# Kernel tuning notes

Measured on AMD Instinct MI355X. Metric: run time of the kernel, lower is better.

## Reference

```python
import jax, jax.numpy as jnp
import numpy as np

B, N, D, H = 2, 2048, 2048, 16
HD = D // H  # head_dim = 128
EPS = 1e-06

def rmsnorm(x, w, eps=EPS):
    xf = x.astype(jnp.float32)
    y = xf * jax.lax.rsqrt(jnp.mean(xf * xf, axis=-1, keepdims=True) + eps)
    return y.astype(x.dtype) * w

def rope_apply(x, freqs, num_heads):
    # x: [B, S, D]; freqs: [S, 1, HD//2, 2] = (cos, sin) of complex rotation
    b, s, d = x.shape
    hd = d // num_heads
    xr = x.reshape(b, s, num_heads, hd // 2, 2)
    x0, x1 = xr[..., 0], xr[..., 1]
    fr, fi = freqs[..., 0], freqs[..., 1]  # broadcast [S,1,HD//2] over heads
    out = jnp.stack([x0 * fr - x1 * fi, x0 * fi + x1 * fr], axis=-1)
    return out.reshape(b, s, d).astype(x.dtype)

def attention(q, k, v, num_heads):
    b, s, d = q.shape
    hd = d // num_heads
    qh = q.reshape(b, s, num_heads, hd).transpose(0, 2, 1, 3)  # b h s d
    kh = k.reshape(b, s, num_heads, hd).transpose(0, 2, 1, 3)
    vh = v.reshape(b, s, num_heads, hd).transpose(0, 2, 1, 3)
    scale = hd ** -0.5
    scores = jnp.einsum('bhqd,bhkd->bhqk', qh, kh) * scale
    probs = jax.nn.softmax(scores, axis=-1)
    out = jnp.einsum('bhqk,bhkd->bhqd', probs, vh)
    return out.transpose(0, 2, 1, 3).reshape(b, s, d)

def setup_inputs() -> dict:
    key = jax.random.key(0)
    ks = jax.random.split(key, 8)
    x = jax.random.normal(ks[0], (B, N, D), jnp.float32)
    # standard RoPE frequencies
    pos = jnp.arange(N, dtype=jnp.float32)
    inv = 1.0 / (10000.0 ** (jnp.arange(0, HD, 2, dtype=jnp.float32) / HD))
    ang = pos[:, None] * inv[None, :]  # [N, HD//2]
    freqs = jnp.stack([jnp.cos(ang), jnp.sin(ang)], axis=-1)[:, None, :, :]  # [N,1,HD//2,2]
    s = 0.02
    wq = jax.random.normal(ks[1], (D, D), jnp.float32) * s
    wk = jax.random.normal(ks[2], (D, D), jnp.float32) * s
    wv = jax.random.normal(ks[3], (D, D), jnp.float32) * s
    wo = jax.random.normal(ks[4], (D, D), jnp.float32) * s
    bq = jnp.zeros((D,), jnp.float32)
    bk = jnp.zeros((D,), jnp.float32)
    bv = jnp.zeros((D,), jnp.float32)
    bo = jnp.zeros((D,), jnp.float32)
    gq = jnp.ones((D,), jnp.float32)
    gk = jnp.ones((D,), jnp.float32)
    return {"x": x, "freqs": freqs, "wq": wq, "bq": bq, "wk": wk, "bk": bk,
            "wv": wv, "bv": bv, "wo": wo, "bo": bo, "gq": gq, "gk": gk}

def reference(x, freqs, wq, bq, wk, bk, wv, bv, wo, bo, gq, gk):
    q = rmsnorm(x @ wq.T + bq, gq)
    k = rmsnorm(x @ wk.T + bk, gk)
    v = x @ wv.T + bv
    q = rope_apply(q, freqs, H)
    k = rope_apply(k, freqs, H)
    attn_out = attention(q, k, v, H)
    return attn_out @ wo.T + bo
```

## Files before the change

kernel.cpp:

```cpp
#include <hip/hip_runtime.h>
#include <hip/hip_bf16.h>
#include <stdint.h>


typedef __bf16 bf16;
typedef __bf16 bf16x8 __attribute__((ext_vector_type(8)));
typedef __bf16 bf16x4 __attribute__((ext_vector_type(4)));
typedef float  f32x4  __attribute__((ext_vector_type(4)));

#define MTOT   4096
#define DMODEL 2048
#define NSEQ   2048
#define NHEAD  16
#define HDIM   128
#define BK     64

static __device__ __forceinline__ void async_ld16(const void* g, void* l) {
  void* gnc = const_cast<void*>(g);
  __builtin_amdgcn_global_load_lds((__attribute__((address_space(1))) void*)gnc,
                                   (__attribute__((address_space(3))) void*)l,
                                   16, 0, 0);
}

__global__ __launch_bounds__(256) void k_cvt(const float* __restrict__ in,
                                             bf16* __restrict__ out, int n8) {
  int stride = gridDim.x * blockDim.x;
  for (int i = blockIdx.x * blockDim.x + threadIdx.x; i < n8; i += stride) {
    const float4* p = (const float4*)(in) + 2 * (size_t)i;
    float4 a = p[0], b = p[1];
    bf16x8 o;
    o[0] = (bf16)a.x; o[1] = (bf16)a.y; o[2] = (bf16)a.z; o[3] = (bf16)a.w;
    o[4] = (bf16)b.x; o[5] = (bf16)b.y; o[6] = (bf16)b.z; o[7] = (bf16)b.w;
    *((bf16x8*)(out) + i) = o;
  }
}

template <int OUTMODE>
static __device__ __forceinline__ void gemm_body(
    const bf16* __restrict__ A, const bf16* __restrict__ W,
    const float* __restrict__ bias, void* __restrict__ outp,
    int m0, int n0, bf16* sa, bf16* sb) {
  const int tid = threadIdx.x;
  const int lane = tid & 63;
  const int w = tid >> 6;
  const int wr = w >> 1, wc = w & 1;
  const int g = lane >> 4, r0 = lane & 15;

  f32x4 acc[4][4];
  const f32x4 vzero = {0.f, 0.f, 0.f, 0.f};
#pragma unroll
  for (int i = 0; i < 4; ++i)
#pragma unroll
    for (int j = 0; j < 4; ++j) acc[i][j] = vzero;

  const bf16* Abase = A + (size_t)m0 * DMODEL;
  const bf16* Wbase = W + (size_t)n0 * DMODEL;

  for (int kt = 0; kt < DMODEL / BK; ++kt) {
    const bf16* asrc = Abase + kt * BK;
    const bf16* bsrc = Wbase + kt * BK;
#pragma unroll
    for (int p = 0; p < 4; ++p) {
      int ch = tid + p * 256;
      int row = ch >> 3, cs = ch & 7;
      int c = cs ^ (row & 7);
      async_ld16(asrc + (size_t)row * DMODEL + c * 8, sa + ch * 8);
    }
#pragma unroll
    for (int p = 0; p < 4; ++p) {
      int ch = tid + p * 256;
      int row = ch >> 3, cs = ch & 7;
      int c = cs ^ (row & 7);
      async_ld16(bsrc + (size_t)row * DMODEL + c * 8, sb + ch * 8);
    }
    asm volatile("s_waitcnt vmcnt(0)" ::: "memory");
    __syncthreads();
#pragma unroll
    for (int ks = 0; ks < 2; ++ks) {
      bf16x8 af[4], bfr[4];
      int c = ks * 4 + g;
#pragma unroll
      for (int i = 0; i < 4; ++i) {
        int ra = wr * 64 + i * 16 + r0;
        af[i] = *(const bf16x8*)(sa + ra * BK + ((c ^ (ra & 7)) << 3));
        int rb = wc * 64 + i * 16 + r0;
        bfr[i] = *(const bf16x8*)(sb + rb * BK + ((c ^ (rb & 7)) << 3));
      }
#pragma unroll
      for (int i = 0; i < 4; ++i)
#pragma unroll
        for (int j = 0; j < 4; ++j)
          acc[i][j] = __builtin_amdgcn_mfma_f32_16x16x32_bf16(af[i], bfr[j],
                                                              acc[i][j], 0, 0, 0);
    }
    __syncthreads();
  }

#pragma unroll
  for (int i = 0; i < 4; ++i) {
#pragma unroll
    for (int j = 0; j < 4; ++j) {
      int mb = m0 + wr * 64 + i * 16 + g * 4;
      int n = n0 + wc * 64 + j * 16 + r0;
      float bn = bias[n];
      if (OUTMODE == 0) {
        bf16* o = (bf16*)outp;
#pragma unroll
        for (int r = 0; r < 4; ++r)
          o[(size_t)(mb + r) * DMODEL + n] = (bf16)(acc[i][j][r] + bn);
      } else if (OUTMODE == 2) {
        float* o = (float*)outp;
#pragma unroll
        for (int r = 0; r < 4; ++r)
          o[(size_t)(mb + r) * DMODEL + n] = acc[i][j][r] + bn;
      } else {
        bf16* o = (bf16*)outp;
        int bb = mb >> 11, s = mb & (NSEQ - 1);
        bf16x4 pk;
#pragma unroll
        for (int r = 0; r < 4; ++r) pk[r] = (bf16)(acc[i][j][r] + bn);
        *(bf16x4*)(o + (size_t)(bb * DMODEL + n) * NSEQ + s) = pk;
      }
    }
  }
}

__global__ __launch_bounds__(256) void k_gemm_qkv(
    const bf16* __restrict__ xb, const bf16* __restrict__ wq,
    const bf16* __restrict__ wk, const bf16* __restrict__ wv,
    const float* __restrict__ bq, const float* __restrict__ bk,
    const float* __restrict__ bv, bf16* __restrict__ q, bf16* __restrict__ k,
    bf16* __restrict__ vt) {
  __shared__ __align__(16) bf16 smem[2 * 128 * BK];
  int nb = blockIdx.x;
  int m0 = blockIdx.y * 128;
  int sec = nb >> 4;
  int n0 = (nb & 15) * 128;
  if (sec == 0)
    gemm_body<0>(xb, wq, bq, q, m0, n0, smem, smem + 128 * BK);
  else if (sec == 1)
    gemm_body<0>(xb, wk, bk, k, m0, n0, smem, smem + 128 * BK);
  else
    gemm_body<1>(xb, wv, bv, vt, m0, n0, smem, smem + 128 * BK);
}

__global__ __launch_bounds__(256) void k_gemm_out(
    const bf16* __restrict__ ab, const bf16* __restrict__ wo,
    const float* __restrict__ bo, float* __restrict__ out) {
  __shared__ __align__(16) bf16 smem[2 * 128 * BK];
  gemm_body<2>(ab, wo, bo, out, blockIdx.y * 128, blockIdx.x * 128, smem,
               smem + 128 * BK);
}

__global__ __launch_bounds__(256) void k_norm_rope(
    bf16* __restrict__ q, bf16* __restrict__ kk, const float* __restrict__ gq,
    const float* __restrict__ gk, const float* __restrict__ freqs) {
  int bidx = blockIdx.x;
  bf16* buf = (bidx < MTOT) ? q : kk;
  const float* gw = (bidx < MTOT) ? gq : gk;
  float qs = (bidx < MTOT) ? 0.08838834764831845f : 1.0f;
  int row = bidx & (MTOT - 1);
  int s = row & (NSEQ - 1);
  int tid = threadIdx.x;
  int i0 = tid * 8;
  bf16* ptr = buf + (size_t)row * DMODEL + i0;
  bf16x8 v = *(const bf16x8*)ptr;
  float x[8];
  float ssq = 0.f;
#pragma unroll
  for (int j = 0; j < 8; ++j) {
    x[j] = (float)v[j];
    ssq += x[j] * x[j];
  }
#pragma unroll
  for (int off = 1; off < 64; off <<= 1) ssq += __shfl_xor(ssq, off);
  __shared__ float part[4];
  if ((tid & 63) == 0) part[tid >> 6] = ssq;
  __syncthreads();
  float tot = part[0] + part[1] + part[2] + part[3];
  float sc = rsqrtf(tot * (1.f / DMODEL) + 1e-6f) * qs;
  float4 g0 = *(const float4*)(gw + i0);
  float4 g1 = *(const float4*)(gw + i0 + 4);
  float y[8];
  y[0] = x[0] * sc * g0.x; y[1] = x[1] * sc * g0.y;
  y[2] = x[2] * sc * g0.z; y[3] = x[3] * sc * g0.w;
  y[4] = x[4] * sc * g1.x; y[5] = x[5] * sc * g1.y;
  y[6] = x[6] * sc * g1.z; y[7] = x[7] * sc * g1.w;
  int dl = i0 & (HDIM - 1);
  const float* fp = freqs + (size_t)s * HDIM + dl;
  float4 f0 = *(const float4*)fp;
  float4 f1 = *(const float4*)(fp + 4);
  bf16x8 out;
  out[0] = (bf16)(y[0] * f0.x - y[1] * f0.y);
  out[1] = (bf16)(y[0] * f0.y + y[1] * f0.x);
  out[2] = (bf16)(y[2] * f0.z - y[3] * f0.w);
  out[3] = (bf16)(y[2] * f0.w + y[3] * f0.z);
  out[4] = (bf16)(y[4] * f1.x - y[5] * f1.y);
  out[5] = (bf16)(y[4] * f1.y + y[5] * f1.x);
  out[6] = (bf16)(y[6] * f1.z - y[7] * f1.w);
  out[7] = (bf16)(y[6] * f1.w + y[7] * f1.z);
  *(bf16x8*)ptr = out;
}

__global__ __launch_bounds__(512, 4) void k_attn(const bf16* __restrict__ q,
                                                 const bf16* __restrict__ k,
                                                 const bf16* __restrict__ vt,
                                                 bf16* __restrict__ o) {
  __shared__ __align__(16) bf16 sk[2][64 * 128];
  __shared__ __align__(16) bf16 sv[2][128 * 64];
  const int bid = blockIdx.x;
  const int idx = bid >> 3;
  const int bh = (bid & 7) * 4 + (idx >> 4);
  const int qt = idx & 15;
  const int bb = bh >> 4, h = bh & 15;
  const int tid = threadIdx.x;
  const int lane = tid & 63, w = tid >> 6;
  const int g = lane >> 4, r0 = lane & 15;

  bf16x8 qf[4];
  {
    const bf16* qbase =
        q + (size_t)(bb * NSEQ + qt * 128 + w * 16 + r0) * DMODEL + h * HDIM;
#pragma unroll
    for (int ds = 0; ds < 4; ++ds)
      qf[ds] = *(const bf16x8*)(qbase + ds * 32 + g * 8);
  }
  f32x4 oacc[8];
  const f32x4 vzero = {0.f, 0.f, 0.f, 0.f};
#pragma unroll
  for (int dt = 0; dt < 8; ++dt) oacc[dt] = vzero;
  float m = -3.0e38f, l = 0.f;

  const bf16* kbase = k + (size_t)(bb * NSEQ) * DMODEL + h * HDIM;
  const bf16* vbase = vt + (size_t)(bb * DMODEL + h * HDIM) * NSEQ;

  const int s0lane = ((lane & 16) << 1) | r0;
  const int s1lane = s0lane | 16;
  const bool hi5 = (lane & 32) != 0;

  auto stage = [&](int t, int buf) {
    int k0 = t * 64;
#pragma unroll
    for (int p = 0; p < 2; ++p) {
      int ch = tid + p * 512;
      int row = ch >> 4, cs = ch & 15;
      int c = cs ^ (row & 7);
      async_ld16(kbase + (size_t)(k0 + row) * DMODEL + c * 8, &sk[buf][ch * 8]);
    }
#pragma unroll
    for (int p = 0; p < 2; ++p) {
      int ch = tid + p * 512;
      int row = ch >> 3, cs = ch & 7;
      int c = cs ^ (row & 7);
      async_ld16(vbase + (size_t)row * NSEQ + k0 + c * 8, &sv[buf][ch * 8]);
    }
  };

  stage(0, 0);
  for (int t = 0; t < NSEQ / 64; ++t) {
    const int cur = t & 1;
    asm volatile("s_waitcnt vmcnt(0)" ::: "memory");
    __syncthreads();
    if (t + 1 < NSEQ / 64) stage(t + 1, cur ^ 1);

    f32x4 sacc[4];
#pragma unroll
    for (int kkt = 0; kkt < 4; ++kkt) sacc[kkt] = vzero;
#pragma unroll
    for (int kkt = 0; kkt < 4; ++kkt) {
      int rk = kkt * 16 + r0;
#pragma unroll
      for (int ds = 0; ds < 4; ++ds) {
        int c = ds * 4 + g;
        bf16x8 kf = *(const bf16x8*)(&sk[cur][rk * 128 + ((c ^ (rk & 7)) << 3)]);
        sacc[kkt] =
            __builtin_amdgcn_mfma_f32_16x16x32_bf16(kf, qf[ds], sacc[kkt], 0, 0, 0);
      }
    }

    float pm = sacc[0][0];
#pragma unroll
    for (int kkt = 0; kkt < 4; ++kkt)
#pragma unroll
      for (int r = 0; r < 4; ++r) pm = fmaxf(pm, sacc[kkt][r]);
    pm = fmaxf(pm, __shfl_xor(pm, 16));
    pm = fmaxf(pm, __shfl_xor(pm, 32));
    const int need = __any(pm > m);
    const float mu = need ? fmaxf(m, pm) : m;

    uint32_t W[4][2];
    float rs = 0.f;
#pragma unroll
    for (int kkt = 0; kkt < 4; ++kkt) {
      float p0 = __expf(sacc[kkt][0] - mu);
      float p1 = __expf(sacc[kkt][1] - mu);
      float p2 = __expf(sacc[kkt][2] - mu);
      float p3 = __expf(sacc[kkt][3] - mu);
      rs += (p0 + p1) + (p2 + p3);
      asm("v_cvt_pk_bf16_f32 %0, %1, %2" : "=v"(W[kkt][0]) : "v"(p0), "v"(p1));
      asm("v_cvt_pk_bf16_f32 %0, %1, %2" : "=v"(W[kkt][1]) : "v"(p2), "v"(p3));
    }
    rs += __shfl_xor(rs, 16);
    rs += __shfl_xor(rs, 32);

    if (need) {
      float alpha = __expf(m - mu);
      m = mu;
      l = l * alpha + rs;
      float a4[4];
#pragma unroll
      for (int r = 0; r < 4; ++r)
        a4[r] = __shfl(alpha, (lane & 48) | (g * 4 + r));
#pragma unroll
      for (int dt = 0; dt < 8; ++dt)
#pragma unroll
        for (int r = 0; r < 4; ++r) oacc[dt][r] *= a4[r];
    } else {
      l += rs;
    }

#pragma unroll
    for (int ks = 0; ks < 2; ++ks) {
      union { uint32_t u[4]; bf16x8 v; } pa;
#pragma unroll
      for (int ww = 0; ww < 4; ++ww) {
        int src = (ww < 2) ? s0lane : s1lane;
        int lo = __shfl((int)W[2 * ks][ww & 1], src);
        int hv = __shfl((int)W[2 * ks + 1][ww & 1], src);
        pa.u[ww] = hi5 ? (uint32_t)hv : (uint32_t)lo;
      }
#pragma unroll
      for (int dt = 0; dt < 8; ++dt) {
        int rv = dt * 16 + r0;
        int c = ks * 4 + g;
        bf16x8 vf = *(const bf16x8*)(&sv[cur][rv * 64 + ((c ^ (rv & 7)) << 3)]);
        oacc[dt] =
            __builtin_amdgcn_mfma_f32_16x16x32_bf16(pa.v, vf, oacc[dt], 0, 0, 0);
      }
    }
  }

  float rl[4];
#pragma unroll
  for (int r = 0; r < 4; ++r) {
    float lr = __shfl(l, (lane & 48) | (g * 4 + r));
    rl[r] = 1.f / lr;
  }
  bf16* obase =
      o + (size_t)(bb * NSEQ + qt * 128 + w * 16 + g * 4) * DMODEL + h * HDIM;
#pragma unroll
  for (int dt = 0; dt < 8; ++dt)
#pragma unroll
    for (int r = 0; r < 4; ++r)
      obase[(size_t)r * DMODEL + dt * 16 + r0] = (bf16)(oacc[dt][r] * rl[r]);
}

extern "C" void kernel_launch(void* const* d_in, const int* in_sizes, int n_in,
                              void* d_out, int out_size, void* d_ws,
                              size_t ws_size, hipStream_t stream) {
  (void)in_sizes; (void)n_in; (void)out_size; (void)ws_size;
  const float* x = (const float*)d_in[0];
  const float* freqs = (const float*)d_in[1];
  const float* wq = (const float*)d_in[2];
  const float* bq = (const float*)d_in[3];
  const float* wk = (const float*)d_in[4];
  const float* bk = (const float*)d_in[5];
  const float* wv = (const float*)d_in[6];
  const float* bv = (const float*)d_in[7];
  const float* wo = (const float*)d_in[8];
  const float* bo = (const float*)d_in[9];
  const float* gq = (const float*)d_in[10];
  const float* gk = (const float*)d_in[11];

  char* ws = (char*)d_ws;
  const size_t SZ_TOK = (size_t)MTOT * DMODEL * sizeof(bf16);
  const size_t SZ_W = (size_t)DMODEL * DMODEL * sizeof(bf16);
  bf16* xb = (bf16*)ws;
  bf16* qb = (bf16*)(ws + SZ_TOK);
  bf16* kb = (bf16*)(ws + 2 * SZ_TOK);
  bf16* vtb = (bf16*)(ws + 3 * SZ_TOK);
  bf16* wqb = (bf16*)(ws + 4 * SZ_TOK);
  bf16* wkb = (bf16*)(ws + 4 * SZ_TOK + SZ_W);
  bf16* wvb = (bf16*)(ws + 4 * SZ_TOK + 2 * SZ_W);

  k_cvt<<<2048, 256, 0, stream>>>(x, xb, (MTOT * DMODEL) / 8);
  k_cvt<<<1024, 256, 0, stream>>>(wq, wqb, (DMODEL * DMODEL) / 8);
  k_cvt<<<1024, 256, 0, stream>>>(wk, wkb, (DMODEL * DMODEL) / 8);
  k_cvt<<<1024, 256, 0, stream>>>(wv, wvb, (DMODEL * DMODEL) / 8);

  k_gemm_qkv<<<dim3(48, 32), 256, 0, stream>>>(xb, wqb, wkb, wvb, bq, bk, bv,
                                               qb, kb, vtb);
  k_cvt<<<1024, 256, 0, stream>>>(wo, wqb, (DMODEL * DMODEL) / 8);

  k_norm_rope<<<2 * MTOT, 256, 0, stream>>>(qb, kb, gq, gk, freqs);

  k_attn<<<512, 512, 0, stream>>>(qb, kb, vtb, xb);

  k_gemm_out<<<dim3(16, 32), 256, 0, stream>>>(xb, wqb, bo, (float*)d_out);
}
```

Before: 311.7 us.

## Use double-buffered 128x256 GEMM tiles with 512 threads and fuse conversions

```diff
diff --git a/kernel.cpp b/kernel.cpp
--- a/kernel.cpp
+++ b/kernel.cpp
@@ -13,13 +13,39 @@
 #define NSEQ   2048
 #define NHEAD  16
 #define HDIM   128
-#define BK     64
 
 static __device__ __forceinline__ void async_ld16(const void* g, void* l) {
   void* gnc = const_cast<void*>(g);
   __builtin_amdgcn_global_load_lds((__attribute__((address_space(1))) void*)gnc,
                                    (__attribute__((address_space(3))) void*)l,
                                    16, 0, 0);
+}
+
+#define XG (MTOT * DMODEL / 8)
+#define WG (DMODEL * DMODEL / 8)
+
+__global__ __launch_bounds__(256) void k_cvt4(
+    const float* __restrict__ x, const float* __restrict__ wq,
+    const float* __restrict__ wk, const float* __restrict__ wv,
+    bf16* __restrict__ xb, bf16* __restrict__ wqb, bf16* __restrict__ wkb,
+    bf16* __restrict__ wvb) {
+  int stride = gridDim.x * blockDim.x;
+  for (int i = blockIdx.x * blockDim.x + threadIdx.x; i < XG + 3 * WG;
+       i += stride) {
+    const float* src;
+    bf16* dst;
+    int off;
+    if (i < XG) { src = x; dst = xb; off = i; }
+    else if (i < XG + WG) { src = wq; dst = wqb; off = i - XG; }
+    else if (i < XG + 2 * WG) { src = wk; dst = wkb; off = i - XG - WG; }
+    else { src = wv; dst = wvb; off = i - XG - 2 * WG; }
+    const float4* p = (const float4*)(src) + 2 * (size_t)off;
+    float4 a = p[0], b = p[1];
+    bf16x8 o;
+    o[0] = (bf16)a.x; o[1] = (bf16)a.y; o[2] = (bf16)a.z; o[3] = (bf16)a.w;
+    o[4] = (bf16)b.x; o[5] = (bf16)b.y; o[6] = (bf16)b.z; o[7] = (bf16)b.w;
+    *((bf16x8*)(dst) + off) = o;
+  }
 }
 
 __global__ __launch_bounds__(256) void k_cvt(const float* __restrict__ in,
@@ -36,14 +62,16 @@
 }
 
 template <int OUTMODE>
-static __device__ __forceinline__ void gemm_body(
+static __device__ __forceinline__ void gemm256_body(
     const bf16* __restrict__ A, const bf16* __restrict__ W,
-    const float* __restrict__ bias, void* __restrict__ outp,
-    int m0, int n0, bf16* sa, bf16* sb) {
+    const float* __restrict__ bias, void* __restrict__ outp, int m0, int n0) {
+  extern __shared__ __align__(16) bf16 dynls[];
+  bf16* sa = dynls;
+  bf16* sb = dynls + 2 * 128 * 64;
+
   const int tid = threadIdx.x;
-  const int lane = tid & 63;
-  const int w = tid >> 6;
-  const int wr = w >> 1, wc = w & 1;
+  const int lane = tid & 63, w = tid >> 6;
+  const int wm = w >> 2, wn = w & 3;
   const int g = lane >> 4, r0 = lane & 15;
 
   f32x4 acc[4][4];
@@ -56,52 +84,74 @@
   const bf16* Abase = A + (size_t)m0 * DMODEL;
   const bf16* Wbase = W + (size_t)n0 * DMODEL;
 
-  for (int kt = 0; kt < DMODEL / BK; ++kt) {
-    const bf16* asrc = Abase + kt * BK;
-    const bf16* bsrc = Wbase + kt * BK;
+  auto stage = [&](int kt, int buf) {
+    const bf16* asrc = Abase + kt * 64;
+    const bf16* bsrc = Wbase + kt * 64;
+    bf16* sA = sa + buf * (128 * 64);
+    bf16* sB = sb + buf * (256 * 64);
+#pragma unroll
+    for (int p = 0; p < 2; ++p) {
+      int ch = tid + p * 512;
+      int row = ch >> 3, cs = ch & 7, c = cs ^ (row & 7);
+      async_ld16(asrc + (size_t)row * DMODEL + c * 8, sA + ch * 8);
+    }
 #pragma unroll
     for (int p = 0; p < 4; ++p) {
-      int ch = tid + p * 256;
-      int row = ch >> 3, cs = ch & 7;
-      int c = cs ^ (row & 7);
-      async_ld16(asrc + (size_t)row * DMODEL + c * 8, sa + ch * 8);
-    }
-#pragma unroll
-    for (int p = 0; p < 4; ++p) {
-      int ch = tid + p * 256;
-      int row = ch >> 3, cs = ch & 7;
-      int c = cs ^ (row & 7);
-      async_ld16(bsrc + (size_t)row * DMODEL + c * 8, sb + ch * 8);
-    }
-    asm volatile("s_waitcnt vmcnt(0)" ::: "memory");
+      int ch = tid + p * 512;
+      int row = ch >> 3, cs = ch & 7, c = cs ^ (row & 7);
+      async_ld16(bsrc + (size_t)row * DMODEL + c * 8, sB + ch * 8);
+    }
+  };
+
+  const int NT = DMODEL / 64;
+  stage(0, 0);
+  for (int kt = 0; kt < NT; ++kt) {
+    const int cb = kt & 1;
     __syncthreads();
-#pragma unroll
-    for (int ks = 0; ks < 2; ++ks) {
-      bf16x8 af[4], bfr[4];
-      int c = ks * 4 + g;
-#pragma unroll
-      for (int i = 0; i < 4; ++i) {
-        int ra = wr * 64 + i * 16 + r0;
-        af[i] = *(const bf16x8*)(sa + ra * BK + ((c ^ (ra & 7)) << 3));
-        int rb = wc * 64 + i * 16 + r0;
-        bfr[i] = *(const bf16x8*)(sb + rb * BK + ((c ^ (rb & 7)) << 3));
+    if (kt + 1 < NT) {
+      stage(kt + 1, cb ^ 1);
+      asm volatile("s_waitcnt vmcnt(6)" ::: "memory");
+    } else {
+      asm volatile("s_waitcnt vmcnt(0)" ::: "memory");
+    }
+    __syncthreads();
+    const bf16* sA = sa + cb * (128 * 64);
+    const bf16* sB = sb + cb * (256 * 64);
+#pragma unroll
+    for (int q = 0; q < 4; ++q) {
+      const int mq = q >> 1, nq = q & 1;
+      bf16x8 af[2][2], bfr[2][2];
+#pragma unroll
+      for (int d = 0; d < 2; ++d) {
+        int ra = wm * 64 + (2 * mq + d) * 16 + r0;
+        int rb = wn * 64 + (2 * nq + d) * 16 + r0;
+#pragma unroll
+        for (int ks = 0; ks < 2; ++ks) {
+          int cc = ks * 4 + g;
+          af[d][ks] = *(const bf16x8*)(sA + ra * 64 + ((cc ^ (ra & 7)) << 3));
+          bfr[d][ks] = *(const bf16x8*)(sB + rb * 64 + ((cc ^ (rb & 7)) << 3));
+        }
       }
-#pragma unroll
-      for (int i = 0; i < 4; ++i)
-#pragma unroll
-        for (int j = 0; j < 4; ++j)
-          acc[i][j] = __builtin_amdgcn_mfma_f32_16x16x32_bf16(af[i], bfr[j],
-                                                              acc[i][j], 0, 0, 0);
-    }
-    __syncthreads();
+      __builtin_amdgcn_s_setprio(1);
+#pragma unroll
+      for (int di = 0; di < 2; ++di)
+#pragma unroll
+        for (int dj = 0; dj < 2; ++dj)
+#pragma unroll
+          for (int ks = 0; ks < 2; ++ks)
+            acc[2 * mq + di][2 * nq + dj] = __builtin_amdgcn_mfma_f32_16x16x32_bf16(
+                af[di][ks], bfr[dj][ks], acc[2 * mq + di][2 * nq + dj], 0, 0, 0);
+      __builtin_amdgcn_s_setprio(0);
+      __builtin_amdgcn_sched_barrier(0);
+    }
   }
 
 #pragma unroll
   for (int i = 0; i < 4; ++i) {
 #pragma unroll
     for (int j = 0; j < 4; ++j) {
-      int mb = m0 + wr * 64 + i * 16 + g * 4;
-      int n = n0 + wc * 64 + j * 16 + r0;
+      int mb = m0 + wm * 64 + i * 16 + g * 4;
+      int n = n0 + wn * 64 + j * 16 + r0;
       float bn = bias[n];
       if (OUTMODE == 0) {
         bf16* o = (bf16*)outp;
@@ -125,31 +175,28 @@
   }
 }
 
-__global__ __launch_bounds__(256) void k_gemm_qkv(
+__global__ __launch_bounds__(512, 2) void k_gemm_qkv(
     const bf16* __restrict__ xb, const bf16* __restrict__ wq,
     const bf16* __restrict__ wk, const bf16* __restrict__ wv,
     const float* __restrict__ bq, const float* __restrict__ bk,
     const float* __restrict__ bv, bf16* __restrict__ q, bf16* __restrict__ k,
     bf16* __restrict__ vt) {
-  __shared__ __align__(16) bf16 smem[2 * 128 * BK];
   int nb = blockIdx.x;
   int m0 = blockIdx.y * 128;
-  int sec = nb >> 4;
-  int n0 = (nb & 15) * 128;
+  int sec = nb >> 3;
+  int n0 = (nb & 7) * 256;
   if (sec == 0)
-    gemm_body<0>(xb, wq, bq, q, m0, n0, smem, smem + 128 * BK);
+    gemm256_body<0>(xb, wq, bq, q, m0, n0);
   else if (sec == 1)
-    gemm_body<0>(xb, wk, bk, k, m0, n0, smem, smem + 128 * BK);
+    gemm256_body<0>(xb, wk, bk, k, m0, n0);
   else
-    gemm_body<1>(xb, wv, bv, vt, m0, n0, smem, smem + 128 * BK);
-}
-
-__global__ __launch_bounds__(256) void k_gemm_out(
+    gemm256_body<1>(xb, wv, bv, vt, m0, n0);
+}
+
+__global__ __launch_bounds__(512, 2) void k_gemm_out(
     const bf16* __restrict__ ab, const bf16* __restrict__ wo,
     const float* __restrict__ bo, float* __restrict__ out) {
-  __shared__ __align__(16) bf16 smem[2 * 128 * BK];
-  gemm_body<2>(ab, wo, bo, out, blockIdx.y * 128, blockIdx.x * 128, smem,
-               smem + 128 * BK);
+  gemm256_body<2>(ab, wo, bo, out, blockIdx.y * 128, blockIdx.x * 256);
 }
 
 __global__ __launch_bounds__(256) void k_norm_rope(
@@ -383,18 +430,24 @@
   bf16* wkb = (bf16*)(ws + 4 * SZ_TOK + SZ_W);
   bf16* wvb = (bf16*)(ws + 4 * SZ_TOK + 2 * SZ_W);
 
-  k_cvt<<<2048, 256, 0, stream>>>(x, xb, (MTOT * DMODEL) / 8);
-  k_cvt<<<1024, 256, 0, stream>>>(wq, wqb, (DMODEL * DMODEL) / 8);
-  k_cvt<<<1024, 256, 0, stream>>>(wk, wkb, (DMODEL * DMODEL) / 8);
-  k_cvt<<<1024, 256, 0, stream>>>(wv, wvb, (DMODEL * DMODEL) / 8);
-
-  k_gemm_qkv<<<dim3(48, 32), 256, 0, stream>>>(xb, wqb, wkb, wvb, bq, bk, bv,
-                                               qb, kb, vtb);
+  static bool attr_done = false;
+  if (!attr_done) {
+    hipFuncSetAttribute((const void*)k_gemm_qkv,
+                        hipFuncAttributeMaxDynamicSharedMemorySize, 98304);
+    hipFuncSetAttribute((const void*)k_gemm_out,
+                        hipFuncAttributeMaxDynamicSharedMemorySize, 98304);
+    attr_done = true;
+  }
+
+  k_cvt4<<<2048, 256, 0, stream>>>(x, wq, wk, wv, xb, wqb, wkb, wvb);
+
+  k_gemm_qkv<<<dim3(24, 32), 512, 98304, stream>>>(xb, wqb, wkb, wvb, bq, bk,
+                                                   bv, qb, kb, vtb);
   k_cvt<<<1024, 256, 0, stream>>>(wo, wqb, (DMODEL * DMODEL) / 8);
 
   k_norm_rope<<<2 * MTOT, 256, 0, stream>>>(qb, kb, gq, gk, freqs);
 
   k_attn<<<512, 512, 0, stream>>>(qb, kb, vtb, xb);
 
-  k_gemm_out<<<dim3(16, 32), 256, 0, stream>>>(xb, wqb, bo, (float*)d_out);
-}
+  k_gemm_out<<<dim3(8, 32), 512, 98304, stream>>>(xb, wqb, bo, (float*)d_out);
+}
```

Result: slower. 350.1 us (+12.3%).
